# Kernel optimization log

Hardware: AMD Instinct MI355X
Metric: run time of the kernel (lower is better)

Reference implementation:

```python
import jax, jax.numpy as jnp
import numpy as np

EPS_LN = 1e-5
W_SCALE = -0.6065306597126334  # -exp(-0.5), fla rwkv7 log-decay soft clamp

def layer_norm(x, w, b):
    m = x.mean(-1, keepdims=True)
    v = x.var(-1, keepdims=True)
    return (x - m) * jax.lax.rsqrt(v + EPS_LN) * w + b

def token_shift(x):
    # shift right by one along time; zero initial state (cache=None path)
    return jnp.pad(x, ((0, 0), (1, 0), (0, 0)))[:, :-1]

def reference(x, pre_w, pre_b, attn_w, attn_b, ffn_w, ffn_b,
              x_r, x_w, x_k, x_v, x_a, x_g,
              W_r, W_k, W_v, W_o,
              w1, w2, w_b, a1, a2, a_b, g1, g2,
              k_k, k_a, r_k, gn_w, gn_b,
              ffn_x_k, W_key, W_val):
    B, T, H = x.shape
    NH, HD = r_k.shape  # heads, head_dim

    # ---- RWKV7Block: first layer pre-norm + attn branch ----
    hidden = layer_norm(x, pre_w, pre_b)
    residual = hidden
    hs = layer_norm(hidden, attn_w, attn_b)

    delta = token_shift(hs) - hs
    xr = hs + delta * x_r
    xw = hs + delta * x_w
    xk = hs + delta * x_k
    xv = hs + delta * x_v
    xa = hs + delta * x_a
    xg = hs + delta * x_g

    r = xr @ W_r
    w_log = W_SCALE * jax.nn.sigmoid(jnp.tanh(xw @ w1) @ w2 + w_b)  # log decay in (-exp(-0.5), 0)
    k = xk @ W_k
    v = xv @ W_v
    # layer_idx == 0 -> v_first = v (no v-lora mixing)
    a = jax.nn.sigmoid((xa @ a1) @ a2 + a_b)          # in-context lr
    g = jax.nn.sigmoid(xg @ g1) @ g2                  # output gate

    kkh = (k * k_k).reshape(B, T, NH, HD)
    kk = kkh / jnp.maximum(jnp.linalg.norm(kkh, axis=-1, keepdims=True), 1e-12)
    k = k * (1.0 + (a - 1.0) * k_a)

    r_h = r.reshape(B, T, NH, HD)
    k_h = k.reshape(B, T, NH, HD)
    v_h = v.reshape(B, T, NH, HD)
    a_h = a.reshape(B, T, NH, HD)
    decay = jnp.exp(w_log).reshape(B, T, NH, HD)
    a_vec = -kk             # removal direction
    b_vec = kk * a_h        # replacement direction

    # ---- delta-rule recurrence: S_t = S * diag(decay) + b (a^T S) + k v^T; o_t = r^T S ----
    def tfirst(t):
        return jnp.moveaxis(t, 1, 0)  # [T, B, NH, HD]
    xs = tuple(map(tfirst, (r_h, decay, k_h, v_h, a_vec, b_vec)))
    S0 = jnp.zeros((B, NH, HD, HD), x.dtype)  # state [key, value]

    def step(S, inp):
        r_t, d_t, k_t, v_t, at, bt = inp
        sa = jnp.einsum('bhk,bhkv->bhv', at, S)
        S = S * d_t[..., None] + bt[..., None] * sa[:, :, None, :] + k_t[..., None] * v_t[:, :, None, :]
        return S, jnp.einsum('bhk,bhkv->bhv', r_t, S)

    _, o = jax.lax.scan(step, S0, xs)
    o = jnp.moveaxis(o, 0, 1)  # [B, T, NH, HD]

    # per-head group norm (fla GroupNorm, eps = head_dim * 1e-5)
    mu = o.mean(-1, keepdims=True)
    var = o.var(-1, keepdims=True)
    o = (o - mu) * jax.lax.rsqrt(var + HD * 1e-5)
    o = (o.reshape(B, T, H) * gn_w + gn_b).reshape(B, T, NH, HD)

    # bonus term + gated output projection
    o = o + (r_h * k_h * r_k).sum(-1, keepdims=True) * v_h
    attn_out = (o.reshape(B, T, H) * g) @ W_o

    # ---- channel mix (FFN) branch ----
    hidden = residual + attn_out
    residual2 = hidden
    hs2 = layer_norm(hidden, ffn_w, ffn_b)
    xk2 = hs2 + (token_shift(hs2) - hs2) * ffn_x_k
    ffn_out = jnp.square(jax.nn.relu(xk2 @ W_key)) @ W_val
    return residual2 + ffn_out


def setup_inputs() -> dict:
    B, T, H, NH, HD, FF = 2, 2048, 1024, 16, 64, 4096
    DW, DA, DG = 64, 64, 128  # lora ranks for decay / a / gate
    key = jax.random.key(0)
    ks = iter(jax.random.split(key, 40))
    def nrm(shape, s):
        return jax.random.normal(next(ks), shape, jnp.float32) * s
    def unif(shape):
        return jax.random.uniform(next(ks), shape, dtype=jnp.float32)
    return dict(
        x=nrm((B, T, H), 1.0),
        pre_w=jnp.ones(H), pre_b=jnp.zeros(H),
        attn_w=jnp.ones(H), attn_b=jnp.zeros(H),
        ffn_w=jnp.ones(H), ffn_b=jnp.zeros(H),
        x_r=unif((H,)), x_w=unif((H,)), x_k=unif((H,)),
        x_v=unif((H,)), x_a=unif((H,)), x_g=unif((H,)),
        W_r=nrm((H, H), 0.02), W_k=nrm((H, H), 0.02),
        W_v=nrm((H, H), 0.02), W_o=nrm((H, H), 0.02),
        w1=nrm((H, DW), 0.02), w2=nrm((DW, H), 0.02), w_b=jnp.zeros(H),
        a1=nrm((H, DA), 0.02), a2=nrm((DA, H), 0.02), a_b=jnp.zeros(H),
        g1=nrm((H, DG), 0.02), g2=nrm((DG, H), 0.02),
        k_k=unif((H,)), k_a=unif((H,)), r_k=nrm((NH, HD), 0.02),
        gn_w=jnp.ones(H), gn_b=jnp.zeros(H),
        ffn_x_k=unif((H,)), W_key=nrm((H, FF), 0.02), W_val=nrm((FF, H), 0.02),
    )
```

## Files before the change

kernel.cpp:

```cpp
#include <hip/hip_runtime.h>
#include <hip/hip_bf16.h>
#include <cstdint>

typedef unsigned short u16;
typedef unsigned short us8 __attribute__((ext_vector_type(8)));
typedef __bf16 bf16x8 __attribute__((ext_vector_type(8)));
typedef float f32x4 __attribute__((ext_vector_type(4)));
typedef uint32_t u32x2 __attribute__((ext_vector_type(2)));
typedef uint32_t u32x4v __attribute__((ext_vector_type(4)));

__device__ __forceinline__ float b2f(u16 u) {
    union { float f; uint32_t i; } x; x.i = ((uint32_t)u) << 16; return x.f;
}
__device__ __forceinline__ u16 f2b(float f) {
    uint32_t u = __float_as_uint(f);
    uint32_t r = (u + 0x7FFFu + ((u >> 16) & 1u)) >> 16;
    return (u16)r;
}
__device__ __forceinline__ float sigm(float x) { return 1.0f / (1.0f + __expf(-x)); }
__device__ __forceinline__ float ldv(const void* p, size_t i, int dt) {
    return dt ? b2f(((const u16*)p)[i]) : ((const float*)p)[i];
}

__device__ __forceinline__ float wave_sum(float v) {
#pragma unroll
    for (int o = 32; o > 0; o >>= 1) v += __shfl_xor(v, o, 64);
    return v;
}
__device__ __forceinline__ void block_reduce2(float& a, float& b, float* sm) {
    int tid = threadIdx.x, wid = tid >> 6, lane = tid & 63;
    float as = wave_sum(a), bs = wave_sum(b);
    __syncthreads();
    if (lane == 0) { sm[wid] = as; sm[8 + wid] = bs; }
    __syncthreads();
    a = sm[0] + sm[1] + sm[2] + sm[3];
    b = sm[8] + sm[9] + sm[10] + sm[11];
}

__device__ __forceinline__ float dpp_sum64(float x) {
    x += __int_as_float(__builtin_amdgcn_update_dpp(0, __float_as_int(x), 0x111, 0xf, 0xf, true));
    x += __int_as_float(__builtin_amdgcn_update_dpp(0, __float_as_int(x), 0x112, 0xf, 0xf, true));
    x += __int_as_float(__builtin_amdgcn_update_dpp(0, __float_as_int(x), 0x114, 0xf, 0xf, true));
    x += __int_as_float(__builtin_amdgcn_update_dpp(0, __float_as_int(x), 0x118, 0xf, 0xf, true));
    x += __int_as_float(__builtin_amdgcn_update_dpp(0, __float_as_int(x), 0x142, 0xa, 0xf, true));
    x += __int_as_float(__builtin_amdgcn_update_dpp(0, __float_as_int(x), 0x143, 0xc, 0xf, true));
    return x;
}

#define DPP1(x, ctrl, rm, bm) \
    x += __int_as_float(__builtin_amdgcn_update_dpp(0, __float_as_int(x), ctrl, rm, bm, true));
__device__ __forceinline__ void dpp_sum64_x4(float& a, float& b, float& c, float& d) {
#define RND(ctrl, rm, bm) \
    DPP1(a, ctrl, rm, bm) DPP1(b, ctrl, rm, bm) DPP1(c, ctrl, rm, bm) DPP1(d, ctrl, rm, bm)
    RND(0x111, 0xf, 0xf)
    RND(0x112, 0xf, 0xf)
    RND(0x114, 0xf, 0xf)
    RND(0x118, 0xf, 0xf)
    RND(0x142, 0xa, 0xf)
    RND(0x143, 0xc, 0xf)
#undef RND
}

__global__ void k_probe(const u16* __restrict__ a0, const u16* __restrict__ a1,
                        const u16* __restrict__ a2, int* __restrict__ hdr) {
    __shared__ int wcnt;
    __shared__ float part[256];
    __shared__ float mag[3];
    int tid = threadIdx.x;
    if (tid == 0) wcnt = 0;
    __syncthreads();
    const u16* arr[3] = { a0, a1, a2 };
    int wild = 0;
    for (int s = 0; s < 3; ++s)
        for (int i = tid; i < 4096; i += 256) {
            u16 u = arr[s][i];
            int e = (u >> 7) & 0xFF;
            float av = fabsf(b2f(u));
            if (e == 0xFF || av > 100.f) wild++;
        }
    atomicAdd(&wcnt, wild);
    __syncthreads();
    int dt = (wcnt < 96) ? 1 : 0;
    for (int s = 0; s < 3; ++s) {
        float m = 0.f;
        if (dt) { for (int i = tid; i < 4096; i += 256) m += fabsf(b2f(arr[s][i])); }
        else    { const float* f = (const float*)arr[s];
                  for (int i = tid; i < 2048; i += 256) m += fabsf(f[i]); }
        part[tid] = m; __syncthreads();
        if (tid == 0) { float t = 0; for (int i = 0; i < 256; ++i) t += part[i]; mag[s] = t; }
        __syncthreads();
    }
    if (tid == 0) {
        int xs = 0;
        if (mag[1] > mag[xs]) xs = 1;
        if (mag[2] > mag[xs]) xs = 2;
        hdr[0] = dt; hdr[1] = xs;
    }
}

__global__ __launch_bounds__(256) void k_ln_in(
    const void* __restrict__ xa, const void* __restrict__ xb, const void* __restrict__ xc,
    const void* __restrict__ pw, const void* __restrict__ pb,
    const void* __restrict__ aw, const void* __restrict__ ab,
    u16* __restrict__ resid, u16* __restrict__ hs, const int* __restrict__ hdr)
{
    __shared__ float sm[16];
    const int dt = hdr[0], xs = hdr[1];
    const void* x = (xs == 0) ? xa : (xs == 1 ? xb : xc);
    int tok = blockIdx.x, tid = threadIdx.x;
    int c = tid * 4;
    size_t off = (size_t)tok * 1024 + c;
    float v0, v1, v2, v3;
    if (dt) {
        ushort4 xv = *(const ushort4*)((const u16*)x + off);
        v0 = b2f(xv.x); v1 = b2f(xv.y); v2 = b2f(xv.z); v3 = b2f(xv.w);
    } else {
        float4 xv = *(const float4*)((const float*)x + off);
        v0 = xv.x; v1 = xv.y; v2 = xv.z; v3 = xv.w;
    }
    float s = v0 + v1 + v2 + v3;
    float q = v0*v0 + v1*v1 + v2*v2 + v3*v3;
    block_reduce2(s, q, sm);
    float mean = s * (1.f/1024.f);
    float var  = q * (1.f/1024.f) - mean*mean;
    float rs = rsqrtf(var + 1e-5f);
    float h0 = (v0-mean)*rs*ldv(pw,c+0,dt) + ldv(pb,c+0,dt);
    float h1 = (v1-mean)*rs*ldv(pw,c+1,dt) + ldv(pb,c+1,dt);
    float h2 = (v2-mean)*rs*ldv(pw,c+2,dt) + ldv(pb,c+2,dt);
    float h3 = (v3-mean)*rs*ldv(pw,c+3,dt) + ldv(pb,c+3,dt);
    ushort4 rv; rv.x = f2b(h0); rv.y = f2b(h1); rv.z = f2b(h2); rv.w = f2b(h3);
    *(ushort4*)(resid + off) = rv;
    float s2 = h0 + h1 + h2 + h3;
    float q2 = h0*h0 + h1*h1 + h2*h2 + h3*h3;
    block_reduce2(s2, q2, sm);
    float m2 = s2 * (1.f/1024.f);
    float vr2 = q2 * (1.f/1024.f) - m2*m2;
    float rs2 = rsqrtf(vr2 + 1e-5f);
    ushort4 o;
    o.x = f2b((h0-m2)*rs2*ldv(aw,c+0,dt) + ldv(ab,c+0,dt));
    o.y = f2b((h1-m2)*rs2*ldv(aw,c+1,dt) + ldv(ab,c+1,dt));
    o.z = f2b((h2-m2)*rs2*ldv(aw,c+2,dt) + ldv(ab,c+2,dt));
    o.w = f2b((h3-m2)*rs2*ldv(aw,c+3,dt) + ldv(ab,c+3,dt));
    *(ushort4*)(hs + off) = o;
}

__global__ __launch_bounds__(256) void k_ln_bf(
    const u16* __restrict__ in, const void* __restrict__ w, const void* __restrict__ b,
    u16* __restrict__ out, const int* __restrict__ hdr)
{
    __shared__ float sm[16];
    const int dt = hdr[0];
    int tok = blockIdx.x, tid = threadIdx.x;
    int c = tid * 4;
    size_t off = (size_t)tok * 1024 + c;
    ushort4 xv = *(const ushort4*)(in + off);
    float v0 = b2f(xv.x), v1 = b2f(xv.y), v2 = b2f(xv.z), v3 = b2f(xv.w);
    float s = v0 + v1 + v2 + v3;
    float q = v0*v0 + v1*v1 + v2*v2 + v3*v3;
    block_reduce2(s, q, sm);
    float mean = s * (1.f/1024.f);
    float var  = q * (1.f/1024.f) - mean*mean;
    float rs = rsqrtf(var + 1e-5f);
    ushort4 o;
    o.x = f2b((v0-mean)*rs*ldv(w,c+0,dt) + ldv(b,c+0,dt));
    o.y = f2b((v1-mean)*rs*ldv(w,c+1,dt) + ldv(b,c+1,dt));
    o.z = f2b((v2-mean)*rs*ldv(w,c+2,dt) + ldv(b,c+2,dt));
    o.w = f2b((v3-mean)*rs*ldv(w,c+3,dt) + ldv(b,c+3,dt));
    *(ushort4*)(out + off) = o;
}

__global__ __launch_bounds__(256) void k_tr(
    const void* __restrict__ W, int K, int N, u16* __restrict__ WT,
    const int* __restrict__ hdr)
{
    const int dt = hdr[0];
    __shared__ u16 t[32][33];
    int n0 = blockIdx.x * 32, k0 = blockIdx.y * 32;
    int tx = threadIdx.x & 31, ty = threadIdx.x >> 5;
#pragma unroll
    for (int r = 0; r < 32; r += 8) {
        int k = k0 + ty + r;
        t[ty + r][tx] = f2b(ldv(W, (size_t)k * N + n0 + tx, dt));
    }
    __syncthreads();
#pragma unroll
    for (int r = 0; r < 32; r += 8) {
        int n = n0 + ty + r;
        WT[(size_t)n * K + k0 + tx] = t[tx][ty + r];
    }
}

__device__ __forceinline__ void mf_epi(
    void* D, int ldd, int mode, const void* bias,
    const u16* add, int ldadd, int dt,
    int row, int col, float v)
{
    size_t di = (size_t)row * ldd + col;
    if (mode == 6) {
        ((float*)D)[di] = v + b2f(add[(size_t)row * ldadd + col]);
        return;
    }
    float rr;
    switch (mode) {
        default: rr = v; break;
        case 2: rr = tanhf(v); break;
        case 3: rr = sigm(v); break;
        case 4: rr = __expf(-0.6065306597126334f * sigm(v + ldv(bias, col, dt))); break;
        case 5: rr = sigm(v + ldv(bias, col, dt)); break;
        case 7: { float t = fmaxf(v, 0.f); rr = t * t; } break;
        case 8: rr = v + b2f(add[(size_t)row * ldadd + col]); break;
    }
    ((u16*)D)[di] = f2b(rr);
}

__global__ __launch_bounds__(256, 2) void k_mf(
    const u16* __restrict__ A, int lda, const void* __restrict__ mixc,
    const u16* __restrict__ BT,
    void* __restrict__ D, int ldd,
    int K, int mode,
    const void* __restrict__ bias,
    const u16* __restrict__ add, int ldadd, const int* __restrict__ hdr)
{
    __shared__ u16 As[128 * 40];
    __shared__ u16 Bs[128 * 40];
    const int dt = hdr[0];
    const int tid = threadIdx.x;
    const int m0 = blockIdx.y * 128, n0 = blockIdx.x * 128;
    const int wid = tid >> 6, lane = tid & 63;
    const int wr = wid >> 1, wc = wid & 1;
    const int lg = lane >> 4, lc = lane & 15;
    const int srow = tid >> 1, shalf = tid & 1;

    f32x4 acc[4][4];
#pragma unroll
    for (int i = 0; i < 4; ++i)
#pragma unroll
        for (int j = 0; j < 4; ++j) acc[i][j] = (f32x4)0.f;

    for (int kb = 0; kb < K; kb += 32) {
        {
            int gr = m0 + srow;
            const u16* ap = A + (size_t)gr * lda + kb + 16 * shalf;
            us8 c1 = *(const us8*)ap;
            us8 c2 = *(const us8*)(ap + 8);
            if (mixc) {
                const u16* pp = ap - ((gr & 2047) ? lda : 0);
                float pz = (gr & 2047) ? 1.f : 0.f;
                us8 p1 = *(const us8*)pp;
                us8 p2 = *(const us8*)(pp + 8);
                int kbase = kb + 16 * shalf;
#pragma unroll
                for (int e = 0; e < 8; ++e) {
                    float cu1 = b2f(c1[e]), cu2 = b2f(c2[e]);
                    c1[e] = f2b(cu1 + (pz * b2f(p1[e]) - cu1) * ldv(mixc, kbase + e, dt));
                    c2[e] = f2b(cu2 + (pz * b2f(p2[e]) - cu2) * ldv(mixc, kbase + 8 + e, dt));
                }
            }
            u16* dst = As + srow * 40 + 16 * shalf;
            *(us8*)dst = c1;
            *(us8*)(dst + 8) = c2;
        }
        {
            const u16* bp = BT + (size_t)(n0 + srow) * K + kb + 16 * shalf;
            u16* dst = Bs + srow * 40 + 16 * shalf;
            *(us8*)dst = *(const us8*)bp;
            *(us8*)(dst + 8) = *(const us8*)(bp + 8);
        }
        __syncthreads();
        bf16x8 af[4], bf[4];
#pragma unroll
        for (int fm = 0; fm < 4; ++fm) {
            const u16* p = As + (wr * 64 + fm * 16 + lc) * 40 + lg * 8;
            union { us8 s; bf16x8 v; } u;
            u.s = *(const us8*)p;
            af[fm] = u.v;
        }
#pragma unroll
        for (int fc = 0; fc < 4; ++fc) {
            const u16* p = Bs + (wc * 64 + fc * 16 + lc) * 40 + lg * 8;
            union { us8 s; bf16x8 v; } u;
            u.s = *(const us8*)p;
            bf[fc] = u.v;
        }
#pragma unroll
        for (int fm = 0; fm < 4; ++fm)
#pragma unroll
            for (int fc = 0; fc < 4; ++fc)
                acc[fm][fc] = __builtin_amdgcn_mfma_f32_16x16x32_bf16(
                    af[fm], bf[fc], acc[fm][fc], 0, 0, 0);
        __syncthreads();
    }

#pragma unroll
    for (int fm = 0; fm < 4; ++fm)
#pragma unroll
        for (int fc = 0; fc < 4; ++fc)
#pragma unroll
            for (int r = 0; r < 4; ++r)
                mf_epi(D, ldd, mode, bias, add, ldadd, dt,
                       m0 + wr * 64 + fm * 16 + lg * 4 + r,
                       n0 + wc * 64 + fc * 16 + lc, acc[fm][fc][r]);
}

__global__ __launch_bounds__(256, 4) void k_mf64(
    const u16* __restrict__ A, int lda, const void* __restrict__ mixc,
    const u16* __restrict__ BT,
    void* __restrict__ D, int ldd,
    int K, int mode,
    const void* __restrict__ bias,
    const u16* __restrict__ add, int ldadd, const int* __restrict__ hdr)
{
    __shared__ u16 As[64 * 40];
    __shared__ u16 Bs[64 * 40];
    const int dt = hdr[0];
    const int tid = threadIdx.x;
    const int m0 = blockIdx.y * 64, n0 = blockIdx.x * 64;
    const int wid = tid >> 6, lane = tid & 63;
    const int wr = wid >> 1, wc = wid & 1;
    const int lg = lane >> 4, lc = lane & 15;
    const int srow = tid >> 2, sq = tid & 3;

    f32x4 acc[2][2];
#pragma unroll
    for (int i = 0; i < 2; ++i)
#pragma unroll
        for (int j = 0; j < 2; ++j) acc[i][j] = (f32x4)0.f;

    for (int kb = 0; kb < K; kb += 32) {
        {
            int gr = m0 + srow;
            const u16* ap = A + (size_t)gr * lda + kb + 8 * sq;
            us8 c1 = *(const us8*)ap;
            if (mixc) {
                const u16* pp = ap - ((gr & 2047) ? lda : 0);
                float pz = (gr & 2047) ? 1.f : 0.f;
                us8 p1 = *(const us8*)pp;
                int kbase = kb + 8 * sq;
#pragma unroll
                for (int e = 0; e < 8; ++e) {
                    float cu = b2f(c1[e]);
                    c1[e] = f2b(cu + (pz * b2f(p1[e]) - cu) * ldv(mixc, kbase + e, dt));
                }
            }
            *(us8*)(As + srow * 40 + 8 * sq) = c1;
        }
        {
            const u16* bp = BT + (size_t)(n0 + srow) * K + kb + 8 * sq;
            *(us8*)(Bs + srow * 40 + 8 * sq) = *(const us8*)bp;
        }
        __syncthreads();
        bf16x8 af[2], bf[2];
#pragma unroll
        for (int fm = 0; fm < 2; ++fm) {
            const u16* p = As + (wr * 32 + fm * 16 + lc) * 40 + lg * 8;
            union { us8 s; bf16x8 v; } u;
            u.s = *(const us8*)p;
            af[fm] = u.v;
        }
#pragma unroll
        for (int fc = 0; fc < 2; ++fc) {
            const u16* p = Bs + (wc * 32 + fc * 16 + lc) * 40 + lg * 8;
            union { us8 s; bf16x8 v; } u;
            u.s = *(const us8*)p;
            bf[fc] = u.v;
        }
#pragma unroll
        for (int fm = 0; fm < 2; ++fm)
#pragma unroll
            for (int fc = 0; fc < 2; ++fc)
                acc[fm][fc] = __builtin_amdgcn_mfma_f32_16x16x32_bf16(
                    af[fm], bf[fc], acc[fm][fc], 0, 0, 0);
        __syncthreads();
    }

#pragma unroll
    for (int fm = 0; fm < 2; ++fm)
#pragma unroll
        for (int fc = 0; fc < 2; ++fc)
#pragma unroll
            for (int r = 0; r < 4; ++r)
                mf_epi(D, ldd, mode, bias, add, ldadd, dt,
                       m0 + wr * 32 + fm * 16 + lg * 4 + r,
                       n0 + wc * 32 + fc * 16 + lc, acc[fm][fc][r]);
}

__global__ __launch_bounds__(256) void k_prep(
    u16* __restrict__ k_bf, const u16* __restrict__ a_buf,
    const void* __restrict__ k_k, const void* __restrict__ k_a,
    u16* __restrict__ av, u16* __restrict__ bv, const int* __restrict__ hdr)
{
    const int dt = hdr[0];
    int ht = blockIdx.x * 4 + (threadIdx.x >> 6);
    int j = threadIdx.x & 63;
    int tok = ht >> 4, h = ht & 15, n = h * 64 + j;
    size_t idx = (size_t)tok * 1024 + n;
    float kv = b2f(k_bf[idx]);
    float a  = b2f(a_buf[idx]);
    float kk = kv * ldv(k_k, n, dt);
    float ss = wave_sum(kk * kk);
    float den = fmaxf(sqrtf(ss), 1e-12f);
    float kkn = kk / den;
    k_bf[idx] = f2b(kv * (1.f + (a - 1.f) * ldv(k_a, n, dt)));
    av[idx] = f2b(-kkn);
    bv[idx] = f2b(kkn * a);
}

#define KREC_LOADS(T0)                                                          \
    {                                                                           \
        _Pragma("unroll")                                                       \
        for (int it = 0; it < 10; ++it) {                                       \
            const u16* sp = (it < 2) ? r_bf : (it < 4) ? dcy                    \
                          : (it < 6) ? km  : (it < 8) ? av : bv;                \
            int i = ((it & 1) << 8) + tid;                                      \
            int step = i >> 5, dp = i & 31;                                     \
            stg[it] = *(const uint32_t*)(sp +                                   \
                (size_t)(tbase + (T0) + step) * 1024 + h * 64 + dp * 2);        \
        }                                                                       \
        if (tid < 64)                                                           \
            stg[10] = v32[(size_t)(tbase + (T0) + (tid >> 2)) * 512             \
                          + h * 32 + jj0 + (tid & 3)];                          \
    }
#define KREC_WRITES(DST)                                                        \
    {                                                                           \
        u16* b_ = (u16*)&lds[DST][0];                                           \
        _Pragma("unroll")                                                       \
        for (int it = 0; it < 10; ++it) {                                       \
            int s = it >> 1;                                                    \
            int i = ((it & 1) << 8) + tid;                                      \
            int step = i >> 5, dp = i & 31;                                     \
            b_[s * 1280 + (2 * dp) * 20 + step]     = (u16)(stg[it] & 0xFFFFu); \
            b_[s * 1280 + (2 * dp + 1) * 20 + step] = (u16)(stg[it] >> 16);     \
        }                                                                       \
        if (tid < 64) lds[DST][3200 + (tid & 3) * 16 + (tid >> 2)] = stg[10];   \
    }
__device__ __forceinline__ float bfsel(uint32_t u, int hi) {
    return hi ? __uint_as_float(u & 0xFFFF0000u) : __uint_as_float(u << 16);
}
__global__ __launch_bounds__(256) void k_rec(
    const u16* __restrict__ r_bf, const u16* __restrict__ dcy,
    const u16* __restrict__ km, const u16* __restrict__ v_bf,
    const u16* __restrict__ av, const u16* __restrict__ bv,
    u16* __restrict__ o_buf)
{
    const int T = 2048;
    const int tid = threadIdx.x;
    int rq = blockIdx.x & 7, q = blockIdx.x >> 3;
    int wid = tid >> 6, lane = tid & 63;
    int bh = rq * 4 + (q >> 3);
    int jj0 = (q & 7) * 4;
    int jj = jj0 + wid;
    int b = bh >> 4, h = bh & 15;
    int tbase = b * T;
    const uint32_t* v32 = (const uint32_t*)v_bf;
    uint32_t* o32 = (uint32_t*)o_buf;
    size_t oidx = (size_t)tbase * 512 + h * 32 + jj;

    __shared__ uint32_t lds[2][3264];
    uint32_t stg[11];

    KREC_LOADS(0)
    KREC_WRITES(0)
    __syncthreads();

    float S0 = 0.f, S1 = 0.f;
    float pv0 = 0.f, pv1 = 0.f;
    for (int c = 0; c < 128; ++c) {
        int cur = c & 1;
        bool more = (c + 1) < 128;
        if (more) KREC_LOADS((c + 1) * 16)
        const char* lbb = (const char*)&lds[cur][0];
        u32x2 rA[4], dA[4], kA[4], aA[4], bA[4];
        u32x4v vA[4];
#pragma unroll
        for (int qq = 0; qq < 4; ++qq) {
            rA[qq] = *(const u32x2*)(lbb + 0 * 2560 + lane * 40 + qq * 8);
            dA[qq] = *(const u32x2*)(lbb + 1 * 2560 + lane * 40 + qq * 8);
            kA[qq] = *(const u32x2*)(lbb + 2 * 2560 + lane * 40 + qq * 8);
            aA[qq] = *(const u32x2*)(lbb + 3 * 2560 + lane * 40 + qq * 8);
            bA[qq] = *(const u32x2*)(lbb + 4 * 2560 + lane * 40 + qq * 8);
            vA[qq] = *(const u32x4v*)(lbb + 12800 + wid * 64 + qq * 16);
        }
#pragma unroll
        for (int step = 0; step < 16; ++step) {
            const int qq = step >> 2, ee = (step >> 1) & 1, hi = step & 1;
            float rf  = bfsel(rA[qq][ee], hi);
            float df  = bfsel(dA[qq][ee], hi);
            float kf  = bfsel(kA[qq][ee], hi);
            float af  = bfsel(aA[qq][ee], hi);
            float bf_ = bfsel(bA[qq][ee], hi);
            uint32_t vv = vA[qq][step & 3];
            float vf0 = __uint_as_float(vv << 16);
            float vf1 = __uint_as_float(vv & 0xFFFF0000u);
            float m0 = af * S0, m1 = af * S1;
            float q0 = pv0, q1 = pv1;
            dpp_sum64_x4(m0, m1, q0, q1);
            float sa0 = __int_as_float(__builtin_amdgcn_readlane(__float_as_int(m0), 63));
            float sa1 = __int_as_float(__builtin_amdgcn_readlane(__float_as_int(m1), 63));
            if (step > 0 || c > 0) {
                if (lane == 63)
                    o32[oidx] = (uint32_t)f2b(q0) | ((uint32_t)f2b(q1) << 16);
                oidx += 512;
            }
            float X0 = fmaf(kf, vf0, S0 * df);
            float X1 = fmaf(kf, vf1, S1 * df);
            S0 = fmaf(bf_, sa0, X0);
            S1 = fmaf(bf_, sa1, X1);
            pv0 = rf * S0;
            pv1 = rf * S1;
        }
        if (more) KREC_WRITES(cur ^ 1)
        __syncthreads();
    }
    {
        float q0 = pv0, q1 = pv1, z0 = 0.f, z1 = 0.f;
        dpp_sum64_x4(q0, q1, z0, z1);
        if (lane == 63)
            o32[oidx] = (uint32_t)f2b(q0) | ((uint32_t)f2b(q1) << 16);
    }
}

__global__ __launch_bounds__(256) void k_post(
    const u16* __restrict__ o_buf, const u16* __restrict__ r_bf,
    const u16* __restrict__ km, const u16* __restrict__ v_bf,
    const u16* __restrict__ g_buf, const void* __restrict__ r_k,
    const void* __restrict__ gnw, const void* __restrict__ gnb,
    u16* __restrict__ ao, const int* __restrict__ hdr)
{
    const int dt = hdr[0];
    int ht = blockIdx.x * 4 + (threadIdx.x >> 6);
    int j = threadIdx.x & 63;
    int tok = ht >> 4, h = ht & 15, n = h * 64 + j;
    size_t idx = (size_t)tok * 1024 + n;
    float o = b2f(o_buf[idx]);
    float mu = wave_sum(o) * (1.f/64.f);
    float d = o - mu;
    float var = wave_sum(d * d) * (1.f/64.f);
    float og = d * rsqrtf(var + 6.4e-4f) * ldv(gnw, n, dt) + ldv(gnb, n, dt);
    float r = b2f(r_bf[idx]), kmv = b2f(km[idx]), v = b2f(v_bf[idx]);
    float bonus = wave_sum(r * kmv * ldv(r_k, n, dt));
    float val = (og + bonus * v) * b2f(g_buf[idx]);
    ao[idx] = f2b(val);
}

extern "C" void kernel_launch(void* const* d_in, const int* in_sizes, int n_in,
                              void* d_out, int out_size, void* d_ws, size_t ws_size,
                              hipStream_t stream) {
    (void)in_sizes; (void)n_in; (void)out_size; (void)ws_size;
    const void* xP     = d_in[0];
    const void* pre_w  = d_in[1];
    const void* pre_b  = d_in[2];
    const void* attn_w = d_in[3];
    const void* attn_b = d_in[4];
    const void* ffn_w  = d_in[5];
    const void* ffn_b  = d_in[6];
    const void* x_r    = d_in[7];
    const void* x_w    = d_in[8];
    const void* x_k    = d_in[9];
    const void* x_v    = d_in[10];
    const void* x_a    = d_in[11];
    const void* x_g    = d_in[12];
    const void* W_r    = d_in[13];
    const void* W_k    = d_in[14];
    const void* W_v    = d_in[15];
    const void* W_o    = d_in[16];
    const void* w1     = d_in[17];
    const void* w2     = d_in[18];
    const void* w_b    = d_in[19];
    const void* a1     = d_in[20];
    const void* a2     = d_in[21];
    const void* a_b    = d_in[22];
    const void* g1     = d_in[23];
    const void* g2     = d_in[24];
    const void* k_k    = d_in[25];
    const void* k_a    = d_in[26];
    const void* r_k    = d_in[27];
    const void* gn_w   = d_in[28];
    const void* gn_b   = d_in[29];
    const void* ffn_xk = d_in[30];
    const void* WkeyP  = d_in[31];
    const void* WvalP  = d_in[32];

    char* ws = (char*)d_ws;
    const size_t SL = 8388608ull;
    int* hdr    = (int*)(ws + 0);
    u16* hs     = (u16*)(ws + 4096 + SL*0);
    u16* resid1 = (u16*)(ws + 4096 + SL*1);
    u16* dcy    = (u16*)(ws + 4096 + SL*2);
    u16* r_bf   = (u16*)(ws + 4096 + SL*3);
    u16* k_bf   = (u16*)(ws + 4096 + SL*4);
    u16* v_bf   = (u16*)(ws + 4096 + SL*5);
    u16* av_bf  = (u16*)(ws + 4096 + SL*6);
    u16* bv_bf  = (u16*)(ws + 4096 + SL*7);
    u16* a_buf  = (u16*)(ws + 4096 + SL*8);
    u16* g_buf  = (u16*)(ws + 4096 + SL*9);
    u16* tmpw   = (u16*)(ws + 4096 + SL*10);
    u16* tmpa   = (u16*)(ws + 4096 + SL*10 + 524288);
    u16* tmpg   = (u16*)(ws + 4096 + SL*10 + 1048576);
    u16* wT     = (u16*)(ws + 4096 + SL*10 + 2097152);
    u16* o_buf  = a_buf;
    u16* ao_in  = bv_bf;
    u16* hid2   = dcy;
    u16* hs2    = hs;
    u16* ffh    = r_bf;

    dim3 blk(256);
    dim3 gm64(16, 64);
    dim3 g4096(32, 32);
    dim3 t1024(32, 32), tKey(128, 32), tVal(32, 128), t64(32, 2), t128(32, 4);
    dim3 tl64(2, 32), tl128(4, 32);
    k_probe<<<1, blk, 0, stream>>>((const u16*)xP, (const u16*)WkeyP, (const u16*)WvalP, hdr);
    k_ln_in<<<4096, blk, 0, stream>>>(xP, WkeyP, WvalP, pre_w, pre_b, attn_w, attn_b, resid1, hs, hdr);

    k_tr<<<t1024, blk, 0, stream>>>(W_r, 1024, 1024, wT, hdr);
    k_mf64<<<gm64, blk, 0, stream>>>(hs, 1024, x_r, wT, r_bf, 1024, 1024, 1, nullptr, nullptr, 0, hdr);
    k_tr<<<tl64, blk, 0, stream>>>(w1, 1024, 64, wT, hdr);
    k_mf64<<<dim3(1, 64), blk, 0, stream>>>(hs, 1024, x_w, wT, tmpw, 64, 1024, 2, nullptr, nullptr, 0, hdr);
    k_tr<<<t64, blk, 0, stream>>>(w2, 64, 1024, wT, hdr);
    k_mf64<<<gm64, blk, 0, stream>>>(tmpw, 64, nullptr, wT, dcy, 1024, 64, 4, w_b, nullptr, 0, hdr);
    k_tr<<<t1024, blk, 0, stream>>>(W_k, 1024, 1024, wT, hdr);
    k_mf64<<<gm64, blk, 0, stream>>>(hs, 1024, x_k, wT, k_bf, 1024, 1024, 1, nullptr, nullptr, 0, hdr);
    k_tr<<<t1024, blk, 0, stream>>>(W_v, 1024, 1024, wT, hdr);
    k_mf64<<<gm64, blk, 0, stream>>>(hs, 1024, x_v, wT, v_bf, 1024, 1024, 1, nullptr, nullptr, 0, hdr);
    k_tr<<<tl64, blk, 0, stream>>>(a1, 1024, 64, wT, hdr);
    k_mf64<<<dim3(1, 64), blk, 0, stream>>>(hs, 1024, x_a, wT, tmpa, 64, 1024, 1, nullptr, nullptr, 0, hdr);
    k_tr<<<t64, blk, 0, stream>>>(a2, 64, 1024, wT, hdr);
    k_mf64<<<gm64, blk, 0, stream>>>(tmpa, 64, nullptr, wT, a_buf, 1024, 64, 5, a_b, nullptr, 0, hdr);
    k_tr<<<tl128, blk, 0, stream>>>(g1, 1024, 128, wT, hdr);
    k_mf64<<<dim3(2, 64), blk, 0, stream>>>(hs, 1024, x_g, wT, tmpg, 128, 1024, 3, nullptr, nullptr, 0, hdr);
    k_tr<<<t128, blk, 0, stream>>>(g2, 128, 1024, wT, hdr);
    k_mf64<<<gm64, blk, 0, stream>>>(tmpg, 128, nullptr, wT, g_buf, 1024, 128, 1, nullptr, nullptr, 0, hdr);

    k_prep<<<16384, blk, 0, stream>>>(k_bf, a_buf, k_k, k_a, av_bf, bv_bf, hdr);
    k_rec<<<256, blk, 0, stream>>>(r_bf, dcy, k_bf, v_bf, av_bf, bv_bf, o_buf);
    k_post<<<16384, blk, 0, stream>>>(o_buf, r_bf, k_bf, v_bf, g_buf, r_k, gn_w, gn_b, ao_in, hdr);

    k_tr<<<t1024, blk, 0, stream>>>(W_o, 1024, 1024, wT, hdr);
    k_mf64<<<gm64, blk, 0, stream>>>(ao_in, 1024, nullptr, wT, hid2, 1024, 1024, 8, nullptr, resid1, 1024, hdr);

    k_ln_bf<<<4096, blk, 0, stream>>>(hid2, ffn_w, ffn_b, hs2, hdr);
    k_tr<<<tKey, blk, 0, stream>>>(WkeyP, 1024, 4096, wT, hdr);
    k_mf<<<g4096, blk, 0, stream>>>(hs2, 1024, ffn_xk, wT, ffh, 4096, 1024, 7, nullptr, nullptr, 0, hdr);
    k_tr<<<tVal, blk, 0, stream>>>(WvalP, 4096, 1024, wT, hdr);
    k_mf64<<<gm64, blk, 0, stream>>>(ffh, 4096, nullptr, wT, (float*)d_out, 1024, 4096, 6, nullptr, hid2, 1024, hdr);
}
```

Baseline: 1.203 ms.

## Batch weight transposes and group projection GEMMs into fewer launches

Replaces the per-weight transpose kernels with a single k_tr_all launch that transposes Wo, Wr/Wk/Wv and the LoRA weights into separate persistent buffers. The separate r/k/v GEMMs, the three LoRA down-projections and the three LoRA up-projections each become one grouped k_mf64g launch, where each block picks its mix vector, output, K, mode and bias from its column range. This cuts kernel-launch count and serialization of small GEMMs, and improves occupancy for the tiny LoRA GEMMs. It costs per-block selection logic and a larger workspace layout.

```diff
diff --git a/kernel.cpp b/kernel.cpp
--- a/kernel.cpp
+++ b/kernel.cpp
@@ -35,16 +35,6 @@
     __syncthreads();
     a = sm[0] + sm[1] + sm[2] + sm[3];
     b = sm[8] + sm[9] + sm[10] + sm[11];
-}
-
-__device__ __forceinline__ float dpp_sum64(float x) {
-    x += __int_as_float(__builtin_amdgcn_update_dpp(0, __float_as_int(x), 0x111, 0xf, 0xf, true));
-    x += __int_as_float(__builtin_amdgcn_update_dpp(0, __float_as_int(x), 0x112, 0xf, 0xf, true));
-    x += __int_as_float(__builtin_amdgcn_update_dpp(0, __float_as_int(x), 0x114, 0xf, 0xf, true));
-    x += __int_as_float(__builtin_amdgcn_update_dpp(0, __float_as_int(x), 0x118, 0xf, 0xf, true));
-    x += __int_as_float(__builtin_amdgcn_update_dpp(0, __float_as_int(x), 0x142, 0xa, 0xf, true));
-    x += __int_as_float(__builtin_amdgcn_update_dpp(0, __float_as_int(x), 0x143, 0xc, 0xf, true));
-    return x;
 }
 
 #define DPP1(x, ctrl, rm, bm) \
@@ -190,14 +180,59 @@
     }
 }
 
+__global__ __launch_bounds__(256) void k_tr_all(
+    const void* __restrict__ Wo, const void* __restrict__ Wr,
+    const void* __restrict__ Wk, const void* __restrict__ Wv,
+    const void* __restrict__ w1, const void* __restrict__ a1,
+    const void* __restrict__ g1,
+    const void* __restrict__ w2, const void* __restrict__ a2,
+    const void* __restrict__ g2,
+    u16* __restrict__ wTo, u16* __restrict__ wTrkv,
+    u16* __restrict__ BTu, u16* __restrict__ BT2,
+    const int* __restrict__ hdr)
+{
+    int bid = blockIdx.x;
+    const void* W; int Nd, ldwt, xt, yt; u16* dst;
+    if (bid < 4096) {
+        int t = bid & 1023, w = bid >> 10;
+        W = (w == 0) ? Wo : (w == 1) ? Wr : (w == 2) ? Wk : Wv;
+        Nd = 1024; ldwt = 1024;
+        dst = (w == 0) ? wTo : wTrkv + (size_t)(w - 1) * 1024 * 1024;
+        xt = t & 31; yt = t >> 5;
+    } else if (bid < 4352) {
+        int t = bid - 4096;
+        ldwt = 1024;
+        if (t < 64)       { W = w1; dst = BTu;              Nd = 64;  xt = t & 1; yt = t >> 1; }
+        else if (t < 128) { W = a1; dst = BTu + 64 * 1024;  Nd = 64;  t -= 64;  xt = t & 1; yt = t >> 1; }
+        else              { W = g1; dst = BTu + 128 * 1024; Nd = 128; t -= 128; xt = t & 3; yt = t >> 2; }
+    } else {
+        int t = bid - 4352;
+        ldwt = 128; Nd = 1024;
+        if (t < 64)       { W = w2; dst = BT2; xt = t & 31; yt = t >> 5; }
+        else if (t < 128) { W = a2; dst = BT2 + 1024 * 128; t -= 64;  xt = t & 31; yt = t >> 5; }
+        else              { W = g2; dst = BT2 + 2048 * 128; t -= 128; xt = t & 31; yt = t >> 5; }
+    }
+    const int dt = hdr[0];
+    __shared__ u16 tb[32][33];
+    int n0 = xt * 32, k0 = yt * 32;
+    int tx = threadIdx.x & 31, ty = threadIdx.x >> 5;
+#pragma unroll
+    for (int r = 0; r < 32; r += 8)
+        tb[ty + r][tx] = f2b(ldv(W, (size_t)(k0 + ty + r) * Nd + n0 + tx, dt));
+    __syncthreads();
+#pragma unroll
+    for (int r = 0; r < 32; r += 8)
+        dst[(size_t)(n0 + ty + r) * ldwt + k0 + tx] = tb[tx][ty + r];
+}
+
 __device__ __forceinline__ void mf_epi(
     void* D, int ldd, int mode, const void* bias,
     const u16* add, int ldadd, int dt,
-    int row, int col, float v)
-{
-    size_t di = (size_t)row * ldd + col;
+    int row, int colD, int colB, float v)
+{
+    size_t di = (size_t)row * ldd + colD;
     if (mode == 6) {
-        ((float*)D)[di] = v + b2f(add[(size_t)row * ldadd + col]);
+        ((float*)D)[di] = v + b2f(add[(size_t)row * ldadd + colD]);
         return;
     }
     float rr;
@@ -205,10 +240,10 @@
         default: rr = v; break;
         case 2: rr = tanhf(v); break;
         case 3: rr = sigm(v); break;
-        case 4: rr = __expf(-0.6065306597126334f * sigm(v + ldv(bias, col, dt))); break;
-        case 5: rr = sigm(v + ldv(bias, col, dt)); break;
+        case 4: rr = __expf(-0.6065306597126334f * sigm(v + ldv(bias, colB, dt))); break;
+        case 5: rr = sigm(v + ldv(bias, colB, dt)); break;
         case 7: { float t = fmaxf(v, 0.f); rr = t * t; } break;
-        case 8: rr = v + b2f(add[(size_t)row * ldadd + col]); break;
+        case 8: rr = v + b2f(add[(size_t)row * ldadd + colD]); break;
     }
     ((u16*)D)[di] = f2b(rr);
 }
@@ -296,18 +331,24 @@
 #pragma unroll
         for (int fc = 0; fc < 4; ++fc)
 #pragma unroll
-            for (int r = 0; r < 4; ++r)
-                mf_epi(D, ldd, mode, bias, add, ldadd, dt,
-                       m0 + wr * 64 + fm * 16 + lg * 4 + r,
-                       n0 + wc * 64 + fc * 16 + lc, acc[fm][fc][r]);
-}
-
-__global__ __launch_bounds__(256, 4) void k_mf64(
-    const u16* __restrict__ A, int lda, const void* __restrict__ mixc,
-    const u16* __restrict__ BT,
-    void* __restrict__ D, int ldd,
-    int K, int mode,
-    const void* __restrict__ bias,
+            for (int r = 0; r < 4; ++r) {
+                int row = m0 + wr * 64 + fm * 16 + lg * 4 + r;
+                int col = n0 + wc * 64 + fc * 16 + lc;
+                mf_epi(D, ldd, mode, bias, add, ldadd, dt, row, col, col, acc[fm][fc][r]);
+            }
+}
+
+__global__ __launch_bounds__(256, 4) void k_mf64g(
+    const u16* __restrict__ A, int lda,
+    const void* mx0, const void* mx1, const void* mx2,
+    const u16* __restrict__ BT, int ldbt,
+    void* D0, void* D1, void* D2, int ldd,
+    int b1, int b2,
+    int K0, int K1, int K2,
+    int ao0, int ao1, int ao2,
+    int dcb0, int dcb1, int dcb2,
+    int md0, int md1, int md2,
+    const void* bs0, const void* bs1, const void* bs2,
     const u16* __restrict__ add, int ldadd, const int* __restrict__ hdr)
 {
     __shared__ u16 As[64 * 40];
@@ -315,6 +356,15 @@
     const int dt = hdr[0];
     const int tid = threadIdx.x;
     const int m0 = blockIdx.y * 64, n0 = blockIdx.x * 64;
+    const int g = (n0 >= b2) ? 2 : (n0 >= b1) ? 1 : 0;
+    const void* mixc = (g == 0) ? mx0 : (g == 1) ? mx1 : mx2;
+    void* D    = (g == 0) ? D0  : (g == 1) ? D1  : D2;
+    const int Kg   = (g == 0) ? K0  : (g == 1) ? K1  : K2;
+    const int aoff = (g == 0) ? ao0 : (g == 1) ? ao1 : ao2;
+    const int dcb  = (g == 0) ? dcb0: (g == 1) ? dcb1: dcb2;
+    const int mode = (g == 0) ? md0 : (g == 1) ? md1 : md2;
+    const void* bias = (g == 0) ? bs0 : (g == 1) ? bs1 : bs2;
+    const int gbase = (g == 0) ? 0 : (g == 1) ? b1 : b2;
     const int wid = tid >> 6, lane = tid & 63;
     const int wr = wid >> 1, wc = wid & 1;
     const int lg = lane >> 4, lc = lane & 15;
@@ -326,10 +376,10 @@
 #pragma unroll
         for (int j = 0; j < 2; ++j) acc[i][j] = (f32x4)0.f;
 
-    for (int kb = 0; kb < K; kb += 32) {
+    for (int kb = 0; kb < Kg; kb += 32) {
         {
             int gr = m0 + srow;
-            const u16* ap = A + (size_t)gr * lda + kb + 8 * sq;
+            const u16* ap = A + (size_t)gr * lda + aoff + kb + 8 * sq;
             us8 c1 = *(const us8*)ap;
             if (mixc) {
                 const u16* pp = ap - ((gr & 2047) ? lda : 0);
@@ -345,7 +395,7 @@
             *(us8*)(As + srow * 40 + 8 * sq) = c1;
         }
         {
-            const u16* bp = BT + (size_t)(n0 + srow) * K + kb + 8 * sq;
+            const u16* bp = BT + (size_t)(n0 + srow) * ldbt + kb + 8 * sq;
             *(us8*)(Bs + srow * 40 + 8 * sq) = *(const us8*)bp;
         }
         __syncthreads();
@@ -378,10 +428,12 @@
 #pragma unroll
         for (int fc = 0; fc < 2; ++fc)
 #pragma unroll
-            for (int r = 0; r < 4; ++r)
+            for (int r = 0; r < 4; ++r) {
+                int row = m0 + wr * 32 + fm * 16 + lg * 4 + r;
+                int col = n0 + wc * 32 + fc * 16 + lc;
                 mf_epi(D, ldd, mode, bias, add, ldadd, dt,
-                       m0 + wr * 32 + fm * 16 + lg * 4 + r,
-                       n0 + wc * 32 + fc * 16 + lc, acc[fm][fc][r]);
+                       row, col - dcb, col - gbase, acc[fm][fc][r]);
+            }
 }
 
 __global__ __launch_bounds__(256) void k_prep(
@@ -593,10 +645,13 @@
     u16* bv_bf  = (u16*)(ws + 4096 + SL*7);
     u16* a_buf  = (u16*)(ws + 4096 + SL*8);
     u16* g_buf  = (u16*)(ws + 4096 + SL*9);
-    u16* tmpw   = (u16*)(ws + 4096 + SL*10);
-    u16* tmpa   = (u16*)(ws + 4096 + SL*10 + 524288);
-    u16* tmpg   = (u16*)(ws + 4096 + SL*10 + 1048576);
-    u16* wT     = (u16*)(ws + 4096 + SL*10 + 2097152);
+    u16* tmp    = (u16*)(ws + 4096 + SL*10);
+    char* wTB   = ws + 4096 + SL*10 + 2097152;
+    u16* wTo    = (u16*)(wTB);
+    u16* wTrkv  = (u16*)(wTB + 2097152);
+    u16* BTu    = (u16*)(wTB + 8388608);
+    u16* BT2    = (u16*)(wTB + 8912896);
+    u16* wTbig  = (u16*)(wTB);
     u16* o_buf  = a_buf;
     u16* ao_in  = bv_bf;
     u16* hid2   = dcy;
@@ -604,42 +659,43 @@
     u16* ffh    = r_bf;
 
     dim3 blk(256);
-    dim3 gm64(16, 64);
-    dim3 g4096(32, 32);
-    dim3 t1024(32, 32), tKey(128, 32), tVal(32, 128), t64(32, 2), t128(32, 4);
-    dim3 tl64(2, 32), tl128(4, 32);
+    const int HUGE = 1 << 30;
     k_probe<<<1, blk, 0, stream>>>((const u16*)xP, (const u16*)WkeyP, (const u16*)WvalP, hdr);
     k_ln_in<<<4096, blk, 0, stream>>>(xP, WkeyP, WvalP, pre_w, pre_b, attn_w, attn_b, resid1, hs, hdr);
 
-    k_tr<<<t1024, blk, 0, stream>>>(W_r, 1024, 1024, wT, hdr);
-    k_mf64<<<gm64, blk, 0, stream>>>(hs, 1024, x_r, wT, r_bf, 1024, 1024, 1, nullptr, nullptr, 0, hdr);
-    k_tr<<<tl64, blk, 0, stream>>>(w1, 1024, 64, wT, hdr);
-    k_mf64<<<dim3(1, 64), blk, 0, stream>>>(hs, 1024, x_w, wT, tmpw, 64, 1024, 2, nullptr, nullptr, 0, hdr);
-    k_tr<<<t64, blk, 0, stream>>>(w2, 64, 1024, wT, hdr);
-    k_mf64<<<gm64, blk, 0, stream>>>(tmpw, 64, nullptr, wT, dcy, 1024, 64, 4, w_b, nullptr, 0, hdr);
-    k_tr<<<t1024, blk, 0, stream>>>(W_k, 1024, 1024, wT, hdr);
-    k_mf64<<<gm64, blk, 0, stream>>>(hs, 1024, x_k, wT, k_bf, 1024, 1024, 1, nullptr, nullptr, 0, hdr);
-    k_tr<<<t1024, blk, 0, stream>>>(W_v, 1024, 1024, wT, hdr);
-    k_mf64<<<gm64, blk, 0, stream>>>(hs, 1024, x_v, wT, v_bf, 1024, 1024, 1, nullptr, nullptr, 0, hdr);
-    k_tr<<<tl64, blk, 0, stream>>>(a1, 1024, 64, wT, hdr);
-    k_mf64<<<dim3(1, 64), blk, 0, stream>>>(hs, 1024, x_a, wT, tmpa, 64, 1024, 1, nullptr, nullptr, 0, hdr);
-    k_tr<<<t64, blk, 0, stream>>>(a2, 64, 1024, wT, hdr);
-    k_mf64<<<gm64, blk, 0, stream>>>(tmpa, 64, nullptr, wT, a_buf, 1024, 64, 5, a_b, nullptr, 0, hdr);
-    k_tr<<<tl128, blk, 0, stream>>>(g1, 1024, 128, wT, hdr);
-    k_mf64<<<dim3(2, 64), blk, 0, stream>>>(hs, 1024, x_g, wT, tmpg, 128, 1024, 3, nullptr, nullptr, 0, hdr);
-    k_tr<<<t128, blk, 0, stream>>>(g2, 128, 1024, wT, hdr);
-    k_mf64<<<gm64, blk, 0, stream>>>(tmpg, 128, nullptr, wT, g_buf, 1024, 128, 1, nullptr, nullptr, 0, hdr);
+    k_tr_all<<<4608, blk, 0, stream>>>(W_o, W_r, W_k, W_v, w1, a1, g1, w2, a2, g2,
+                                       wTo, wTrkv, BTu, BT2, hdr);
+
+    k_mf64g<<<dim3(48, 64), blk, 0, stream>>>(hs, 1024, x_r, x_k, x_v,
+        wTrkv, 1024, r_bf, k_bf, v_bf, 1024, 1024, 2048,
+        1024, 1024, 1024, 0, 0, 0, 0, 1024, 2048,
+        1, 1, 1, nullptr, nullptr, nullptr, nullptr, 0, hdr);
+
+    k_mf64g<<<dim3(4, 64), blk, 0, stream>>>(hs, 1024, x_w, x_a, x_g,
+        BTu, 1024, tmp, tmp, tmp, 256, 64, 128,
+        1024, 1024, 1024, 0, 0, 0, 0, 0, 0,
+        2, 1, 3, nullptr, nullptr, nullptr, nullptr, 0, hdr);
+
+    k_mf64g<<<dim3(48, 64), blk, 0, stream>>>(tmp, 256, nullptr, nullptr, nullptr,
+        BT2, 128, dcy, a_buf, g_buf, 1024, 1024, 2048,
+        64, 64, 128, 0, 64, 128, 0, 1024, 2048,
+        4, 5, 1, w_b, a_b, nullptr, nullptr, 0, hdr);
 
     k_prep<<<16384, blk, 0, stream>>>(k_bf, a_buf, k_k, k_a, av_bf, bv_bf, hdr);
     k_rec<<<256, blk, 0, stream>>>(r_bf, dcy, k_bf, v_bf, av_bf, bv_bf, o_buf);
     k_post<<<16384, blk, 0, stream>>>(o_buf, r_bf, k_bf, v_bf, g_buf, r_k, gn_w, gn_b, ao_in, hdr);
 
-    k_tr<<<t1024, blk, 0, stream>>>(W_o, 1024, 1024, wT, hdr);
-    k_mf64<<<gm64, blk, 0, stream>>>(ao_in, 1024, nullptr, wT, hid2, 1024, 1024, 8, nullptr, resid1, 1024, hdr);
+    k_mf64g<<<dim3(16, 64), blk, 0, stream>>>(ao_in, 1024, nullptr, nullptr, nullptr,
+        wTo, 1024, hid2, hid2, hid2, 1024, HUGE, HUGE,
+        1024, 1024, 1024, 0, 0, 0, 0, 0, 0,
+        8, 8, 8, nullptr, nullptr, nullptr, resid1, 1024, hdr);
 
     k_ln_bf<<<4096, blk, 0, stream>>>(hid2, ffn_w, ffn_b, hs2, hdr);
-    k_tr<<<tKey, blk, 0, stream>>>(WkeyP, 1024, 4096, wT, hdr);
-    k_mf<<<g4096, blk, 0, stream>>>(hs2, 1024, ffn_xk, wT, ffh, 4096, 1024, 7, nullptr, nullptr, 0, hdr);
-    k_tr<<<tVal, blk, 0, stream>>>(WvalP, 4096, 1024, wT, hdr);
-    k_mf64<<<gm64, blk, 0, stream>>>(ffh, 4096, nullptr, wT, (float*)d_out, 1024, 4096, 6, nullptr, hid2, 1024, hdr);
-}
+    k_tr<<<dim3(128, 32), blk, 0, stream>>>(WkeyP, 1024, 4096, wTbig, hdr);
+    k_mf<<<dim3(32, 32), blk, 0, stream>>>(hs2, 1024, ffn_xk, wTbig, ffh, 4096, 1024, 7, nullptr, nullptr, 0, hdr);
+    k_tr<<<dim3(32, 128), blk, 0, stream>>>(WvalP, 4096, 1024, wTbig, hdr);
+    k_mf64g<<<dim3(16, 64), blk, 0, stream>>>(ffh, 4096, nullptr, nullptr, nullptr,
+        wTbig, 4096, d_out, d_out, d_out, 1024, HUGE, HUGE,
+        4096, 4096, 4096, 0, 0, 0, 0, 0, 0,
+        6, 6, 6, nullptr, nullptr, nullptr, hid2, 1024, hdr);
+}
```

Result: faster. 1.071 ms (-11.0%).
